# Kernel tuning notes

Hardware: AMD Instinct MI355X
Metric: run time of the kernel (lower is better)

The kernel has to match this reference:

```python
import jax, jax.numpy as jnp
import numpy as np

T, B, N, E = 16384, 64, 1_000_000, 4096  # steps, per-step batch, train samples, eval dim


def setup_inputs() -> dict:
    key = jax.random.key(0)
    k1, k2, k3 = jax.random.split(key, 3)
    indices = jax.random.randint(k1, (T, B), 0, N, dtype=jnp.int64)
    M_prev = jax.random.normal(k2, (E,), dtype=jnp.float32)
    # torch module initializes params to zeros; use small random values so the
    # affine recurrence exercises nontrivial math without blowing up.
    params = jax.random.normal(k3, (N, 2), dtype=jnp.float32) * 0.01
    return {"indices": indices, "M_prev": M_prev, "params": params}


def reference(indices, M_prev, params):
    # Per-step gather + sum: alpha_t = sum(params[idx_t, 0]), beta_t = sum(params[idx_t, 1])
    coeffs = params[indices].sum(axis=1)          # [T, 2]
    alpha, beta = coeffs[:, 0], coeffs[:, 1]      # [T], [T]

    # Affine recurrence M_t = alpha_t * M_{t-1} + beta_t as a parallel scan:
    # compose (a1,b1) then (a2,b2) -> (a2*a1, a2*b1 + b2)
    def compose(c1, c2):
        a1, b1 = c1
        a2, b2 = c2
        return a2 * a1, a2 * b1 + b2

    A, Bc = jax.lax.associative_scan(compose, (alpha, beta))  # prefix affine maps
    # M_t = A_t * M_0 + B_t, broadcast over eval dim -> [T, E]
    return A[:, None] * M_prev[None, :] + Bc[:, None]
```

## Files before the change

kernel.cpp:

```cpp
#include <hip/hip_runtime.h>

#define T_DIM 16384
#define B_DIM 64
#define E_DIM 4096
#define NBLK  1024
#define CHUNK 16

typedef float f32x4 __attribute__((ext_vector_type(4)));

__global__ __launch_bounds__(256) void fused_kernel(
    const int*    __restrict__ indices,
    const float*  __restrict__ params,
    const float*  __restrict__ M,
    float*        __restrict__ out,
    float*        __restrict__ aggA,
    float*        __restrict__ aggB,
    unsigned int* __restrict__ flags)
{
    __shared__ float sA[CHUNK], sB[CHUNK];
    __shared__ float sP[2];
    const int tid   = threadIdx.x;
    const int lane  = tid & 63;
    const int wave  = tid >> 6;
    const int blk   = blockIdx.x;
    const int tbase = blk * CHUNK;

    {
        const float2* __restrict__ P2 = (const float2*)params;
        const int j0 = wave * 4;
        int i0 = indices[((tbase + j0 + 0) << 6) + lane];
        int i1 = indices[((tbase + j0 + 1) << 6) + lane];
        int i2 = indices[((tbase + j0 + 2) << 6) + lane];
        int i3 = indices[((tbase + j0 + 3) << 6) + lane];
        float2 p0 = P2[i0], p1 = P2[i1], p2 = P2[i2], p3 = P2[i3];
        float a0 = p0.x, b0 = p0.y, a1 = p1.x, b1 = p1.y;
        float a2 = p2.x, b2 = p2.y, a3 = p3.x, b3 = p3.y;
        #pragma unroll
        for (int off = 32; off >= 1; off >>= 1) {
            a0 += __shfl_down(a0, off, 64);  b0 += __shfl_down(b0, off, 64);
            a1 += __shfl_down(a1, off, 64);  b1 += __shfl_down(b1, off, 64);
            a2 += __shfl_down(a2, off, 64);  b2 += __shfl_down(b2, off, 64);
            a3 += __shfl_down(a3, off, 64);  b3 += __shfl_down(b3, off, 64);
        }
        if (lane == 0) {
            sA[j0+0] = a0; sB[j0+0] = b0;
            sA[j0+1] = a1; sB[j0+1] = b1;
            sA[j0+2] = a2; sB[j0+2] = b2;
            sA[j0+3] = a3; sB[j0+3] = b3;
        }
    }
    __syncthreads();

    if (tid == 0) {
        float a = 1.0f, b = 0.0f;
        #pragma unroll
        for (int j = 0; j < CHUNK; ++j) {
            float aj = sA[j], bj = sB[j];
            b = aj * b + bj;
            a = aj * a;
            sA[j] = a; sB[j] = b;
        }
        __hip_atomic_store(&aggA[blk], a, __ATOMIC_RELAXED, __HIP_MEMORY_SCOPE_AGENT);
        __hip_atomic_store(&aggB[blk], b, __ATOMIC_RELAXED, __HIP_MEMORY_SCOPE_AGENT);
        __hip_atomic_store(&flags[blk], 1u, __ATOMIC_RELEASE, __HIP_MEMORY_SCOPE_AGENT);
    }

    const f32x4* __restrict__ M4 = (const f32x4*)M;
    f32x4 m0 = M4[tid], m1 = M4[tid + 256], m2 = M4[tid + 512], m3 = M4[tid + 768];

    if (wave == 0) {
        float Pa = 1.0f, Pb = 0.0f;
        const int npred   = blk;
        const int nrounds = (npred + 63) >> 6;
        for (int r = 0; r < nrounds; ++r) {
            const int  idx = (r << 6) + lane;
            const bool act = idx < npred;
            const unsigned long long need = __ballot(act);
            for (;;) {
                unsigned int f = act
                    ? __hip_atomic_load(&flags[idx], __ATOMIC_ACQUIRE, __HIP_MEMORY_SCOPE_AGENT)
                    : 1u;
                unsigned long long got = __ballot(f != 0u);
                if ((got & need) == need) break;
                __builtin_amdgcn_s_sleep(1);
            }
            float a = act ? __hip_atomic_load(&aggA[idx], __ATOMIC_RELAXED, __HIP_MEMORY_SCOPE_AGENT) : 1.0f;
            float b = act ? __hip_atomic_load(&aggB[idx], __ATOMIC_RELAXED, __HIP_MEMORY_SCOPE_AGENT) : 0.0f;
            #pragma unroll
            for (int off = 1; off < 64; off <<= 1) {
                float pa = __shfl_up(a, off, 64);
                float pb = __shfl_up(b, off, 64);
                if (lane >= off) {
                    float nb = a * pb + b;
                    a = a * pa;
                    b = nb;
                }
            }
            const float Sa = __shfl(a, 63, 64);
            const float Sb = __shfl(b, 63, 64);
            const float nPb = Sa * Pb + Sb;
            Pa = Sa * Pa;
            Pb = nPb;
        }
        if (lane == 0) { sP[0] = Pa; sP[1] = Pb; }
    }
    __syncthreads();

    const float Pa = sP[0], Pb = sP[1];
    #pragma unroll
    for (int j = 0; j < CHUNK; ++j) {
        const float la = sA[j], lb = sB[j];
        const float At = la * Pa;
        const float Bt = la * Pb + lb;
        f32x4* __restrict__ O4 = (f32x4*)(out + (size_t)(tbase + j) * E_DIM);
        f32x4 r;
        r = At * m0 + Bt;  __builtin_nontemporal_store(r, &O4[tid      ]);
        r = At * m1 + Bt;  __builtin_nontemporal_store(r, &O4[tid + 256]);
        r = At * m2 + Bt;  __builtin_nontemporal_store(r, &O4[tid + 512]);
        r = At * m3 + Bt;  __builtin_nontemporal_store(r, &O4[tid + 768]);
    }
}

extern "C" void kernel_launch(void* const* d_in, const int* in_sizes, int n_in,
                              void* d_out, int out_size, void* d_ws, size_t ws_size,
                              hipStream_t stream) {
    const int*   indices = (const int*)d_in[0];
    const float* M_prev  = (const float*)d_in[1];
    const float* params  = (const float*)d_in[2];
    float* out = (float*)d_out;

    float*        aggA  = (float*)d_ws;
    float*        aggB  = aggA + NBLK;
    unsigned int* flags = (unsigned int*)(aggB + NBLK);

    hipMemsetAsync(flags, 0, NBLK * sizeof(unsigned int), stream);

    fused_kernel<<<NBLK, 256, 0, stream>>>(indices, params, M_prev, out,
                                           aggA, aggB, flags);
}
```

Measured before the change: 353.0 us.

## Use decoupled look-back with inclusive prefixes in cross-block scan

Each block now publishes its inclusive prefix after computing it (flag 2), and the look-back walks backward from the nearest predecessor. It stops at the first window containing a published inclusive prefix instead of reducing all earlier aggregates. This turns the linear-in-block-index aggregate reduction into a short look-back, at the cost of a serial combine loop within the window and extra workspace stores. The launch bounds also request 4 blocks per CU.

```diff
diff --git a/kernel.cpp b/kernel.cpp
--- a/kernel.cpp
+++ b/kernel.cpp
@@ -8,13 +8,17 @@
 
 typedef float f32x4 __attribute__((ext_vector_type(4)));
 
-__global__ __launch_bounds__(256) void fused_kernel(
+#define SCOPE_AGENT __HIP_MEMORY_SCOPE_AGENT
+
+__global__ __launch_bounds__(256, 4) void fused_kernel(
     const int*    __restrict__ indices,
     const float*  __restrict__ params,
     const float*  __restrict__ M,
     float*        __restrict__ out,
     float*        __restrict__ aggA,
     float*        __restrict__ aggB,
+    float*        __restrict__ prefA,
+    float*        __restrict__ prefB,
     unsigned int* __restrict__ flags)
 {
     __shared__ float sA[CHUNK], sB[CHUNK];
@@ -51,6 +55,7 @@
     }
     __syncthreads();
 
+    float own_a = 0.0f, own_b = 0.0f;
     if (tid == 0) {
         float a = 1.0f, b = 0.0f;
         #pragma unroll
@@ -60,49 +65,87 @@
             a = aj * a;
             sA[j] = a; sB[j] = b;
         }
-        __hip_atomic_store(&aggA[blk], a, __ATOMIC_RELAXED, __HIP_MEMORY_SCOPE_AGENT);
-        __hip_atomic_store(&aggB[blk], b, __ATOMIC_RELAXED, __HIP_MEMORY_SCOPE_AGENT);
-        __hip_atomic_store(&flags[blk], 1u, __ATOMIC_RELEASE, __HIP_MEMORY_SCOPE_AGENT);
+        own_a = a; own_b = b;
+        __hip_atomic_store(&aggA[blk], a, __ATOMIC_RELAXED, SCOPE_AGENT);
+        __hip_atomic_store(&aggB[blk], b, __ATOMIC_RELAXED, SCOPE_AGENT);
+        __hip_atomic_store(&flags[blk], 1u, __ATOMIC_RELEASE, SCOPE_AGENT);
     }
 
     const f32x4* __restrict__ M4 = (const f32x4*)M;
     f32x4 m0 = M4[tid], m1 = M4[tid + 256], m2 = M4[tid + 512], m3 = M4[tid + 768];
 
     if (wave == 0) {
-        float Pa = 1.0f, Pb = 0.0f;
-        const int npred   = blk;
-        const int nrounds = (npred + 63) >> 6;
-        for (int r = 0; r < nrounds; ++r) {
-            const int  idx = (r << 6) + lane;
-            const bool act = idx < npred;
-            const unsigned long long need = __ballot(act);
+        float Xa = 1.0f, Xb = 0.0f;
+        float ACCa = 1.0f, ACCb = 0.0f;
+        int  widx = blk - 1;
+        bool done = (widx < 0);
+        while (!done) {
+            const int  base = widx - 63;
+            const int  idx  = base + lane;
+            const bool act  = idx >= 0;
+            float a = 1.0f, b = 0.0f;
+            unsigned fl = 0u;
+            bool have = !act;
             for (;;) {
-                unsigned int f = act
-                    ? __hip_atomic_load(&flags[idx], __ATOMIC_ACQUIRE, __HIP_MEMORY_SCOPE_AGENT)
-                    : 1u;
-                unsigned long long got = __ballot(f != 0u);
-                if ((got & need) == need) break;
-                __builtin_amdgcn_s_sleep(1);
+                if (!have) {
+                    fl = __hip_atomic_load(&flags[idx], __ATOMIC_ACQUIRE, SCOPE_AGENT);
+                    if (fl != 0u) {
+                        if (fl == 2u) {
+                            a = __hip_atomic_load(&prefA[idx], __ATOMIC_RELAXED, SCOPE_AGENT);
+                            b = __hip_atomic_load(&prefB[idx], __ATOMIC_RELAXED, SCOPE_AGENT);
+                        } else {
+                            a = __hip_atomic_load(&aggA[idx], __ATOMIC_RELAXED, SCOPE_AGENT);
+                            b = __hip_atomic_load(&aggB[idx], __ATOMIC_RELAXED, SCOPE_AGENT);
+                        }
+                        have = true;
+                    }
+                }
+                if (__all(have)) break;
+                __builtin_amdgcn_s_sleep(2);
             }
-            float a = act ? __hip_atomic_load(&aggA[idx], __ATOMIC_RELAXED, __HIP_MEMORY_SCOPE_AGENT) : 1.0f;
-            float b = act ? __hip_atomic_load(&aggB[idx], __ATOMIC_RELAXED, __HIP_MEMORY_SCOPE_AGENT) : 0.0f;
-            #pragma unroll
-            for (int off = 1; off < 64; off <<= 1) {
-                float pa = __shfl_up(a, off, 64);
-                float pb = __shfl_up(b, off, 64);
-                if (lane >= off) {
-                    float nb = a * pb + b;
-                    a = a * pa;
-                    b = nb;
+            const unsigned long long m2 = __ballot(act && (fl == 2u));
+            if (m2 != 0ull) {
+                const int L = 63 - __clzll(m2);
+                float Pa = __shfl(a, L, 64);
+                float Pb = __shfl(b, L, 64);
+                for (int s = L + 1; s < 64; ++s) {
+                    const float sa = __shfl(a, s, 64);
+                    const float sb = __shfl(b, s, 64);
+                    Pb = sa * Pb + sb;
+                    Pa = sa * Pa;
                 }
+                Xa = ACCa * Pa;
+                Xb = ACCa * Pb + ACCb;
+                done = true;
+            } else {
+                float ia = a, ib = b;
+                #pragma unroll
+                for (int off = 1; off < 64; off <<= 1) {
+                    const float pa = __shfl_up(ia, off, 64);
+                    const float pb = __shfl_up(ib, off, 64);
+                    if (lane >= off) {
+                        const float nb = ia * pb + ib;
+                        ia = ia * pa;
+                        ib = nb;
+                    }
+                }
+                const float Sa = __shfl(ia, 63, 64);
+                const float Sb = __shfl(ib, 63, 64);
+                const float nb = ACCa * Sb + ACCb;
+                ACCa = ACCa * Sa;
+                ACCb = nb;
+                widx = base - 1;
+                if (widx < 0) { Xa = ACCa; Xb = ACCb; done = true; }
             }
-            const float Sa = __shfl(a, 63, 64);
-            const float Sb = __shfl(b, 63, 64);
-            const float nPb = Sa * Pb + Sb;
-            Pa = Sa * Pa;
-            Pb = nPb;
         }
-        if (lane == 0) { sP[0] = Pa; sP[1] = Pb; }
+        if (lane == 0) {
+            sP[0] = Xa; sP[1] = Xb;
+            const float inc_a = own_a * Xa;
+            const float inc_b = own_a * Xb + own_b;
+            __hip_atomic_store(&prefA[blk], inc_a, __ATOMIC_RELAXED, SCOPE_AGENT);
+            __hip_atomic_store(&prefB[blk], inc_b, __ATOMIC_RELAXED, SCOPE_AGENT);
+            __hip_atomic_store(&flags[blk], 2u, __ATOMIC_RELEASE, SCOPE_AGENT);
+        }
     }
     __syncthreads();
 
@@ -131,10 +174,12 @@
 
     float*        aggA  = (float*)d_ws;
     float*        aggB  = aggA + NBLK;
-    unsigned int* flags = (unsigned int*)(aggB + NBLK);
+    float*        prefA = aggB + NBLK;
+    float*        prefB = prefA + NBLK;
+    unsigned int* flags = (unsigned int*)(prefB + NBLK);
 
     hipMemsetAsync(flags, 0, NBLK * sizeof(unsigned int), stream);
 
     fused_kernel<<<NBLK, 256, 0, stream>>>(indices, params, M_prev, out,
-                                           aggA, aggB, flags);
+                                           aggA, aggB, prefA, prefB, flags);
 }
```

Result: slower. 362.7 us (+2.7%).
